# Kernel optimization log

Measured on AMD Instinct MI355X. Metric: run time of the kernel, lower is better.

Reference implementation:

```python
import jax, jax.numpy as jnp
import numpy as np

N_M, N_D, E, D, H, O = 50000, 20000, 600000, 128, 128, 64


def _graph_conv(x_src, x_dst, src, dst, W_rel, b_rel, W_root, ew=None):
    # PyG GraphConv: lin_rel(scatter_add(msg)) + lin_root(x_dst)
    msg = x_src[src]                       # [E, d_src] gather
    if ew is not None:
        msg = msg * ew[:, None]            # edge-weighted messages
    agg = jax.ops.segment_sum(msg, dst, num_segments=x_dst.shape[0])  # [N_dst, d_src]
    return agg @ W_rel + b_rel + x_dst @ W_root


def setup_inputs() -> dict:
    key = jax.random.key(0)
    ks = jax.random.split(key, 16)
    s = 1.0 / np.sqrt(D)
    inp = {
        "x_meas": jax.random.normal(ks[0], (N_M, D), jnp.float32),
        "x_dem": jax.random.normal(ks[1], (N_D, D), jnp.float32),
        "src_m": jax.random.randint(ks[2], (E,), 0, N_M, jnp.int32),
        "dst_m": jax.random.randint(ks[3], (E,), 0, N_M, jnp.int32),
        "src_b": jax.random.randint(ks[4], (E,), 0, N_M, jnp.int32),
        "dst_b": jax.random.randint(ks[5], (E,), 0, N_D, jnp.int32),
        "edge_weight": jax.random.normal(ks[6], (E,), jnp.float32),
        "W_rel1": jax.random.normal(ks[7], (D, H), jnp.float32) * s,
        "b_rel1": jnp.zeros((H,), jnp.float32),
        "W_root1": jax.random.normal(ks[8], (D, H), jnp.float32) * s,
        "W_rel2": jax.random.normal(ks[9], (D, H), jnp.float32) * s,
        "b_rel2": jnp.zeros((H,), jnp.float32),
        "W_root2": jax.random.normal(ks[10], (D, H), jnp.float32) * s,
        "W_rel3": jax.random.normal(ks[11], (H, H), jnp.float32) * s,
        "b_rel3": jnp.zeros((H,), jnp.float32),
        "W_root3": jax.random.normal(ks[12], (H, H), jnp.float32) * s,
        "W_lin": jax.random.normal(ks[13], (H, O), jnp.float32) * (1.0 / np.sqrt(H)),
        "b_lin": jnp.zeros((O,), jnp.float32),
    }
    return inp


def reference(x_meas, x_dem, src_m, dst_m, src_b, dst_b, edge_weight,
              W_rel1, b_rel1, W_root1, W_rel2, b_rel2, W_root2,
              W_rel3, b_rel3, W_root3, W_lin, b_lin):
    ew = jax.nn.sigmoid(edge_weight)
    movie_x = jax.nn.relu(_graph_conv(x_meas, x_meas, src_m, dst_m, W_rel1, b_rel1, W_root1))
    user_x = jax.nn.relu(_graph_conv(x_meas, x_dem, src_b, dst_b, W_rel2, b_rel2, W_root2, ew))
    user_x = jax.nn.relu(_graph_conv(movie_x, user_x, src_b, dst_b, W_rel3, b_rel3, W_root3, ew))
    return user_x @ W_lin + b_lin  # [N_D, O]
```

## Files before the change

kernel.cpp:

```cpp
#include <hip/hip_runtime.h>


typedef unsigned short u16;
typedef unsigned int u32;
typedef __attribute__((ext_vector_type(8))) short bf16x8;
typedef __attribute__((ext_vector_type(4))) float f32x4;

#define NMC 50000
#define NDC 20000
#define EC  600000
#define CM  64
#define CD  32
#define CHM (EC / CM)
#define CHD (EC / CD)
#define NWM (NMC / 2)
#define NWD (NDC / 2)

__device__ __forceinline__ float bf2f(u16 h) {
    union { u32 u; float f; } v; v.u = ((u32)h) << 16; return v.f;
}
__device__ __forceinline__ u16 f2bf(float f) {
    union { float f; u32 u; } v; v.f = f;
    u32 lsb = (v.u >> 16) & 1u;
    v.u += 0x7fffu + lsb;
    return (u16)(v.u >> 16);
}

__global__ __launch_bounds__(256)
void hist_lds(const int* __restrict__ dst_m, const int* __restrict__ dst_b,
              int* __restrict__ rank_m, int* __restrict__ rank_b,
              u32* __restrict__ histm, u32* __restrict__ histd)
{
    __shared__ u32 h[NWM];
    const int b = blockIdx.x;
    const bool isM = b < CM;
    const int nw = isM ? NWM : NWD;
    for (int i = threadIdx.x; i < nw; i += 256) h[i] = 0;
    __syncthreads();
    if (isM) {
        const int e0 = b * CHM;
        const int e1 = min(EC, e0 + CHM);
        for (int e = e0 + threadIdx.x; e < e1; e += 256) {
            int d = dst_m[e];
            int sh = (d & 1) * 16;
            u32 old = atomicAdd(&h[d >> 1], 1u << sh);
            rank_m[e] = (old >> sh) & 0xffffu;
        }
        __syncthreads();
        for (int i = threadIdx.x; i < nw; i += 256)
            histm[(size_t)b * NWM + i] = h[i];
    } else {
        const int bb = b - CM;
        const int e0 = bb * CHD;
        const int e1 = min(EC, e0 + CHD);
        for (int e = e0 + threadIdx.x; e < e1; e += 256) {
            int d = dst_b[e];
            int sh = (d & 1) * 16;
            u32 old = atomicAdd(&h[d >> 1], 1u << sh);
            rank_b[e] = (old >> sh) & 0xffffu;
        }
        __syncthreads();
        for (int i = threadIdx.x; i < nw; i += 256)
            histd[(size_t)bb * NWD + i] = h[i];
    }
}

__global__ __launch_bounds__(256)
void prep2(const float* __restrict__ xm, u16* __restrict__ xm_bf, int n8m,
           const float* __restrict__ xd, u16* __restrict__ xd_bf, int n8d,
           const float* __restrict__ w0, const float* __restrict__ w1,
           const float* __restrict__ w2, const float* __restrict__ w3,
           const float* __restrict__ w4, const float* __restrict__ w5,
           const float* __restrict__ w6, u16* __restrict__ wbuf,
           int TB, int TB2)
{
    const int b = blockIdx.x;
    if (b < TB + TB2) {
        const bool isM = b < TB;
        const float* src = isM ? xm : xd;
        u16* dst = isM ? xm_bf : xd_bf;
        int n8 = isM ? n8m : n8d;
        int i = (b - (isM ? 0 : TB)) * 256 + threadIdx.x;
        if (i >= n8) return;
        float4 a = ((const float4*)src)[2 * i];
        float4 c2 = ((const float4*)src)[2 * i + 1];
        ushort4 h0; h0.x = f2bf(a.x); h0.y = f2bf(a.y); h0.z = f2bf(a.z); h0.w = f2bf(a.w);
        ushort4 h1; h1.x = f2bf(c2.x); h1.y = f2bf(c2.y); h1.z = f2bf(c2.z); h1.w = f2bf(c2.w);
        ((ushort4*)dst)[2 * i]     = h0;
        ((ushort4*)dst)[2 * i + 1] = h1;
    } else {
        int bb = b - TB - TB2;
        const int widx = bb >> 6;
        const int o    = ((bb & 63) << 8) + threadIdx.x;
        const int OC   = (widx == 6) ? 64 : 128;
        if (o >= OC * 128) return;
        const float* W;
        switch (widx) {
            case 0: W = w0; break; case 1: W = w1; break; case 2: W = w2; break;
            case 3: W = w3; break; case 4: W = w4; break; case 5: W = w5; break;
            default: W = w6;
        }
        int j = o & 7;
        int lane = (o >> 3) & 63;
        int n, c;
        if (OC == 128) { n = (o >> 9) & 7; c = o >> 12; }
        else           { n = (o >> 9) & 3; c = o >> 11; }
        int col = n * 16 + (lane & 15);
        int k   = c * 32 + (lane >> 4) * 8 + j;
        wbuf[widx * 16384 + o] = f2bf(W[k * OC + col]);
    }
}

__global__ __launch_bounds__(256)
void basescan2(u32* __restrict__ histm, u32* __restrict__ histd,
               int* __restrict__ deg_m, int* __restrict__ deg_b)
{
    int w = blockIdx.x * 256 + threadIdx.x;
    u32* hist; int* deg; int NW, C;
    if (w < NWM)            { hist = histm; deg = deg_m; NW = NWM; C = CM; }
    else if (w < NWM + NWD) { hist = histd; deg = deg_b; NW = NWD; C = CD; w -= NWM; }
    else return;
    u32 runlo = 0, runhi = 0;
    for (int c = 0; c < C; ++c) {
        u32 v = hist[(size_t)c * NW + w];
        hist[(size_t)c * NW + w] = runlo | (runhi << 16);
        runlo += v & 0xffffu;
        runhi += v >> 16;
    }
    deg[2 * w]     = (int)runlo;
    deg[2 * w + 1] = (int)runhi;
}

__device__ __forceinline__ int wave_incl_scan(int v, int lane) {
#pragma unroll
    for (int off = 1; off < 64; off <<= 1) {
        int t = __shfl_up(v, off, 64);
        if (lane >= off) v += t;
    }
    return v;
}

__global__ __launch_bounds__(1024)
void scan2_kernel(const int* __restrict__ degA, int* __restrict__ rpA, int nA,
                  const int* __restrict__ degB, int* __restrict__ rpB, int nB)
{
    const int* deg = blockIdx.x ? degB : degA;
    int* rp = blockIdx.x ? rpB : rpA;
    int n = blockIdx.x ? nB : nA;

    __shared__ int wsum[16];
    __shared__ int carry;
    const int tid = threadIdx.x, lane = tid & 63, wid = tid >> 6;
    if (tid == 0) carry = 0;
    __syncthreads();

    for (int base = 0; base < n; base += 4096) {
        int idx = base + tid * 4;
        int4 v = make_int4(0, 0, 0, 0);
        if (idx + 3 < n) v = *(const int4*)(deg + idx);
        else {
            if (idx + 0 < n) v.x = deg[idx + 0];
            if (idx + 1 < n) v.y = deg[idx + 1];
            if (idx + 2 < n) v.z = deg[idx + 2];
            if (idx + 3 < n) v.w = deg[idx + 3];
        }
        int s = v.x + v.y + v.z + v.w;
        int incl = wave_incl_scan(s, lane);
        if (lane == 63) wsum[wid] = incl;
        __syncthreads();
        if (wid == 0) {
            int t = (lane < 16) ? wsum[lane] : 0;
            int ti = wave_incl_scan(t, lane);
            if (lane < 16) wsum[lane] = ti - t;
        }
        __syncthreads();
        int base_t = carry + wsum[wid] + incl - s;
        if (idx + 3 < n) {
            int4 st;
            st.x = base_t;
            st.y = base_t + v.x;
            st.z = base_t + v.x + v.y;
            st.w = base_t + v.x + v.y + v.z;
            *(int4*)(rp + idx) = st;
        } else {
            if (idx + 0 < n) rp[idx + 0] = base_t;
            if (idx + 1 < n) rp[idx + 1] = base_t + v.x;
            if (idx + 2 < n) rp[idx + 2] = base_t + v.x + v.y;
            if (idx + 3 < n) rp[idx + 3] = base_t + v.x + v.y + v.z;
        }
        __syncthreads();
        if (tid == 1023) carry += wsum[15] + incl;
        __syncthreads();
    }
    if (tid == 0) rp[n] = carry;
}

__global__ __launch_bounds__(256)
void fill_kernel(const int* __restrict__ src_m, const int* __restrict__ dst_m,
                 const int* __restrict__ src_b, const int* __restrict__ dst_b,
                 const float* __restrict__ edge_w,
                 const int* __restrict__ rp_m, const int* __restrict__ rp_b,
                 const int* __restrict__ rank_m, const int* __restrict__ rank_b,
                 const u32* __restrict__ histm, const u32* __restrict__ histd,
                 int* __restrict__ srcs_m, int2* __restrict__ edges_b, int E)
{
    int t = blockIdx.x * 256 + threadIdx.x;
    if (t < E) {
        int d = dst_m[t];
        int c = t / CHM;
        u32 pk = histm[(size_t)c * NWM + (d >> 1)];
        int base = (pk >> ((d & 1) * 16)) & 0xffffu;
        int pos = rp_m[d] + base + rank_m[t];
        srcs_m[pos] = src_m[t];
    } else if (t < 2 * E) {
        int e = t - E;
        int d = dst_b[e];
        int c = e / CHD;
        u32 pkb = histd[(size_t)c * NWD + (d >> 1)];
        int base = (pkb >> ((d & 1) * 16)) & 0xffffu;
        int pos = rp_b[d] + base + rank_b[e];
        float x = edge_w[e];
        int2 pk;
        pk.x = src_b[e];
        pk.y = __float_as_int(1.0f / (1.0f + __expf(-x)));
        edges_b[pos] = pk;
    }
}

__global__ __launch_bounds__(256)
void gather12(const u16* __restrict__ Xb,
              const int* __restrict__ srcs_m, const int2* __restrict__ edges_b,
              const int* __restrict__ rp_m, const int* __restrict__ rp_b,
              u16* __restrict__ agg1, u16* __restrict__ agg2, int NM, int ND)
{
    const int h  = blockIdx.x * 8 + (threadIdx.x >> 5);
    const int cl = threadIdx.x & 31;
    float4 acc = make_float4(0.f, 0.f, 0.f, 0.f);

    if (h < NM) {
        int i   = rp_m[h];
        int end = rp_m[h + 1];
        for (; i + 4 <= end; i += 4) {
            int s0 = srcs_m[i], s1 = srcs_m[i + 1], s2 = srcs_m[i + 2], s3 = srcs_m[i + 3];
            ushort4 v0 = *(const ushort4*)(Xb + (size_t)s0 * 128 + cl * 4);
            ushort4 v1 = *(const ushort4*)(Xb + (size_t)s1 * 128 + cl * 4);
            ushort4 v2 = *(const ushort4*)(Xb + (size_t)s2 * 128 + cl * 4);
            ushort4 v3 = *(const ushort4*)(Xb + (size_t)s3 * 128 + cl * 4);
            acc.x += (bf2f(v0.x) + bf2f(v1.x)) + (bf2f(v2.x) + bf2f(v3.x));
            acc.y += (bf2f(v0.y) + bf2f(v1.y)) + (bf2f(v2.y) + bf2f(v3.y));
            acc.z += (bf2f(v0.z) + bf2f(v1.z)) + (bf2f(v2.z) + bf2f(v3.z));
            acc.w += (bf2f(v0.w) + bf2f(v1.w)) + (bf2f(v2.w) + bf2f(v3.w));
        }
        for (; i < end; ++i) {
            int s = srcs_m[i];
            ushort4 v = *(const ushort4*)(Xb + (size_t)s * 128 + cl * 4);
            acc.x += bf2f(v.x); acc.y += bf2f(v.y);
            acc.z += bf2f(v.z); acc.w += bf2f(v.w);
        }
        ushort4 st;
        st.x = f2bf(acc.x); st.y = f2bf(acc.y);
        st.z = f2bf(acc.z); st.w = f2bf(acc.w);
        *(ushort4*)(agg1 + (size_t)h * 128 + cl * 4) = st;
    } else if (h < NM + ND) {
        int node = h - NM;
        int i   = rp_b[node];
        int end = rp_b[node + 1];
        for (; i + 4 <= end; i += 4) {
            int2 p0 = edges_b[i],     p1 = edges_b[i + 1];
            int2 p2 = edges_b[i + 2], p3 = edges_b[i + 3];
            float w0 = __int_as_float(p0.y), w1 = __int_as_float(p1.y);
            float w2 = __int_as_float(p2.y), w3 = __int_as_float(p3.y);
            ushort4 v0 = *(const ushort4*)(Xb + (size_t)p0.x * 128 + cl * 4);
            ushort4 v1 = *(const ushort4*)(Xb + (size_t)p1.x * 128 + cl * 4);
            ushort4 v2 = *(const ushort4*)(Xb + (size_t)p2.x * 128 + cl * 4);
            ushort4 v3 = *(const ushort4*)(Xb + (size_t)p3.x * 128 + cl * 4);
            acc.x = fmaf(w0, bf2f(v0.x), acc.x); acc.y = fmaf(w0, bf2f(v0.y), acc.y);
            acc.z = fmaf(w0, bf2f(v0.z), acc.z); acc.w = fmaf(w0, bf2f(v0.w), acc.w);
            acc.x = fmaf(w1, bf2f(v1.x), acc.x); acc.y = fmaf(w1, bf2f(v1.y), acc.y);
            acc.z = fmaf(w1, bf2f(v1.z), acc.z); acc.w = fmaf(w1, bf2f(v1.w), acc.w);
            acc.x = fmaf(w2, bf2f(v2.x), acc.x); acc.y = fmaf(w2, bf2f(v2.y), acc.y);
            acc.z = fmaf(w2, bf2f(v2.z), acc.z); acc.w = fmaf(w2, bf2f(v2.w), acc.w);
            acc.x = fmaf(w3, bf2f(v3.x), acc.x); acc.y = fmaf(w3, bf2f(v3.y), acc.y);
            acc.z = fmaf(w3, bf2f(v3.z), acc.z); acc.w = fmaf(w3, bf2f(v3.w), acc.w);
        }
        for (; i < end; ++i) {
            int2 pk = edges_b[i];
            float w = __int_as_float(pk.y);
            ushort4 v = *(const ushort4*)(Xb + (size_t)pk.x * 128 + cl * 4);
            acc.x = fmaf(w, bf2f(v.x), acc.x); acc.y = fmaf(w, bf2f(v.y), acc.y);
            acc.z = fmaf(w, bf2f(v.z), acc.z); acc.w = fmaf(w, bf2f(v.w), acc.w);
        }
        ushort4 st;
        st.x = f2bf(acc.x); st.y = f2bf(acc.y);
        st.z = f2bf(acc.z); st.w = f2bf(acc.w);
        *(ushort4*)(agg2 + (size_t)node * 128 + cl * 4) = st;
    }
}

__global__ __launch_bounds__(256)
void gather3_kernel(const u16* __restrict__ Mv, const int2* __restrict__ edges_b,
                    const int* __restrict__ rp_b, u16* __restrict__ agg3, int ND)
{
    const int node = blockIdx.x * 8 + (threadIdx.x >> 5);
    if (node >= ND) return;
    const int cl = threadIdx.x & 31;
    int i   = rp_b[node];
    int end = rp_b[node + 1];

    float4 acc = make_float4(0.f, 0.f, 0.f, 0.f);
    for (; i + 4 <= end; i += 4) {
        int2 p0 = edges_b[i],     p1 = edges_b[i + 1];
        int2 p2 = edges_b[i + 2], p3 = edges_b[i + 3];
        float w0 = __int_as_float(p0.y), w1 = __int_as_float(p1.y);
        float w2 = __int_as_float(p2.y), w3 = __int_as_float(p3.y);
        ushort4 v0 = *(const ushort4*)(Mv + (size_t)p0.x * 128 + cl * 4);
        ushort4 v1 = *(const ushort4*)(Mv + (size_t)p1.x * 128 + cl * 4);
        ushort4 v2 = *(const ushort4*)(Mv + (size_t)p2.x * 128 + cl * 4);
        ushort4 v3 = *(const ushort4*)(Mv + (size_t)p3.x * 128 + cl * 4);
        acc.x = fmaf(w0, bf2f(v0.x), acc.x); acc.y = fmaf(w0, bf2f(v0.y), acc.y);
        acc.z = fmaf(w0, bf2f(v0.z), acc.z); acc.w = fmaf(w0, bf2f(v0.w), acc.w);
        acc.x = fmaf(w1, bf2f(v1.x), acc.x); acc.y = fmaf(w1, bf2f(v1.y), acc.y);
        acc.z = fmaf(w1, bf2f(v1.z), acc.z); acc.w = fmaf(w1, bf2f(v1.w), acc.w);
        acc.x = fmaf(w2, bf2f(v2.x), acc.x); acc.y = fmaf(w2, bf2f(v2.y), acc.y);
        acc.z = fmaf(w2, bf2f(v2.z), acc.z); acc.w = fmaf(w2, bf2f(v2.w), acc.w);
        acc.x = fmaf(w3, bf2f(v3.x), acc.x); acc.y = fmaf(w3, bf2f(v3.y), acc.y);
        acc.z = fmaf(w3, bf2f(v3.z), acc.z); acc.w = fmaf(w3, bf2f(v3.w), acc.w);
    }
    for (; i < end; ++i) {
        int2 pk = edges_b[i];
        float w = __int_as_float(pk.y);
        ushort4 v = *(const ushort4*)(Mv + (size_t)pk.x * 128 + cl * 4);
        acc.x = fmaf(w, bf2f(v.x), acc.x); acc.y = fmaf(w, bf2f(v.y), acc.y);
        acc.z = fmaf(w, bf2f(v.z), acc.z); acc.w = fmaf(w, bf2f(v.w), acc.w);
    }
    ushort4 st;
    st.x = f2bf(acc.x); st.y = f2bf(acc.y);
    st.z = f2bf(acc.z); st.w = f2bf(acc.w);
    *(ushort4*)(agg3 + (size_t)node * 128 + cl * 4) = st;
}

__global__ __launch_bounds__(256)
void conv12_mfma(const u16* __restrict__ agg1, const u16* __restrict__ w1r,
                 const float* __restrict__ b1, const u16* __restrict__ xm_bf,
                 const u16* __restrict__ w1o, u16* __restrict__ C1, int N1, int cb1,
                 const u16* __restrict__ agg2, const u16* __restrict__ w2r,
                 const float* __restrict__ b2, const u16* __restrict__ xd_bf,
                 const u16* __restrict__ w2o, u16* __restrict__ C2, int N2)
{
    __shared__ u16 sW[16384];

    const bool seg1 = (int)blockIdx.x < cb1;
    const u16 *A0, *A1p, *Wr, *Wo; const float* bias; u16* C; int N, base;
    if (seg1) { A0 = agg1; A1p = xm_bf; Wr = w1r; Wo = w1o; bias = b1; C = C1; N = N1; base = blockIdx.x; }
    else      { A0 = agg2; A1p = xd_bf; Wr = w2r; Wo = w2o; bias = b2; C = C2; N = N2; base = blockIdx.x - cb1; }

    const int tid  = threadIdx.x;
    const int lane = tid & 63;
    const int m0   = (base * 4 + (tid >> 6)) * 32;
    const int lr   = lane & 15;
    const int quad = lane >> 4;

    int r0 = m0 + lr;      if (r0 >= N) r0 = N - 1;
    int r1 = m0 + 16 + lr; if (r1 >= N) r1 = N - 1;

    f32x4 acc[2][8];
#pragma unroll
    for (int mt = 0; mt < 2; ++mt)
#pragma unroll
        for (int n = 0; n < 8; ++n) acc[mt][n] = (f32x4){0.f, 0.f, 0.f, 0.f};

    for (int i = tid; i < 2048; i += 256)
        ((uint4*)sW)[i] = ((const uint4*)Wr)[i];
    __syncthreads();
#pragma unroll
    for (int c = 0; c < 4; ++c) {
        const int kb = c * 32 + quad * 8;
        bf16x8 a0 = *(const bf16x8*)(A0 + (size_t)r0 * 128 + kb);
        bf16x8 a1 = *(const bf16x8*)(A0 + (size_t)r1 * 128 + kb);
        const u16* wp = sW + c * 4096 + lane * 8;
#pragma unroll
        for (int n = 0; n < 8; ++n) {
            bf16x8 b = *(const bf16x8*)(wp + n * 512);
            acc[0][n] = __builtin_amdgcn_mfma_f32_16x16x32_bf16(a0, b, acc[0][n], 0, 0, 0);
            acc[1][n] = __builtin_amdgcn_mfma_f32_16x16x32_bf16(a1, b, acc[1][n], 0, 0, 0);
        }
    }
    __syncthreads();

    for (int i = tid; i < 2048; i += 256)
        ((uint4*)sW)[i] = ((const uint4*)Wo)[i];
    __syncthreads();
#pragma unroll
    for (int c = 0; c < 4; ++c) {
        const int kb = c * 32 + quad * 8;
        bf16x8 a0 = *(const bf16x8*)(A1p + (size_t)r0 * 128 + kb);
        bf16x8 a1 = *(const bf16x8*)(A1p + (size_t)r1 * 128 + kb);
        const u16* wp = sW + c * 4096 + lane * 8;
#pragma unroll
        for (int n = 0; n < 8; ++n) {
            bf16x8 b = *(const bf16x8*)(wp + n * 512);
            acc[0][n] = __builtin_amdgcn_mfma_f32_16x16x32_bf16(a0, b, acc[0][n], 0, 0, 0);
            acc[1][n] = __builtin_amdgcn_mfma_f32_16x16x32_bf16(a1, b, acc[1][n], 0, 0, 0);
        }
    }

#pragma unroll
    for (int mt = 0; mt < 2; ++mt) {
#pragma unroll
        for (int n = 0; n < 8; ++n) {
            const int col = n * 16 + lr;
            const float b = bias[col];
#pragma unroll
            for (int r = 0; r < 4; ++r) {
                int row = m0 + mt * 16 + quad * 4 + r;
                if (row >= N) continue;
                C[(size_t)row * 128 + col] = f2bf(fmaxf(acc[mt][n][r] + b, 0.f));
            }
        }
    }
}

__global__ __launch_bounds__(256)
void conv3_lin(const u16* __restrict__ A1, const u16* __restrict__ Wr,
               const float* __restrict__ bias3,
               const u16* __restrict__ A2, const u16* __restrict__ Wo,
               const u16* __restrict__ Wl, const float* __restrict__ bias_l,
               float* __restrict__ out, int N)
{
    __shared__ u16 lds[17408 + 8192];
    u16* tile = lds;
    u16* sWl  = lds + 17408;

    const int tid  = threadIdx.x;
    const int lane = tid & 63;
    const int wv   = tid >> 6;
    const int wbase = wv * 32;
    const int m0   = (blockIdx.x * 4 + wv) * 32;
    const int lr   = lane & 15;
    const int quad = lane >> 4;

    int r0 = m0 + lr;      if (r0 >= N) r0 = N - 1;
    int r1 = m0 + 16 + lr; if (r1 >= N) r1 = N - 1;

    f32x4 acc[2][8];
#pragma unroll
    for (int mt = 0; mt < 2; ++mt)
#pragma unroll
        for (int n = 0; n < 8; ++n) acc[mt][n] = (f32x4){0.f, 0.f, 0.f, 0.f};

    for (int i = tid; i < 1024; i += 256)
        ((uint4*)sWl)[i] = ((const uint4*)Wl)[i];
    for (int i = tid; i < 2048; i += 256)
        ((uint4*)lds)[i] = ((const uint4*)Wr)[i];
    __syncthreads();
#pragma unroll
    for (int c = 0; c < 4; ++c) {
        const int kb = c * 32 + quad * 8;
        bf16x8 a0 = *(const bf16x8*)(A1 + (size_t)r0 * 128 + kb);
        bf16x8 a1 = *(const bf16x8*)(A1 + (size_t)r1 * 128 + kb);
        const u16* wp = lds + c * 4096 + lane * 8;
#pragma unroll
        for (int n = 0; n < 8; ++n) {
            bf16x8 b = *(const bf16x8*)(wp + n * 512);
            acc[0][n] = __builtin_amdgcn_mfma_f32_16x16x32_bf16(a0, b, acc[0][n], 0, 0, 0);
            acc[1][n] = __builtin_amdgcn_mfma_f32_16x16x32_bf16(a1, b, acc[1][n], 0, 0, 0);
        }
    }
    __syncthreads();
    for (int i = tid; i < 2048; i += 256)
        ((uint4*)lds)[i] = ((const uint4*)Wo)[i];
    __syncthreads();
#pragma unroll
    for (int c = 0; c < 4; ++c) {
        const int kb = c * 32 + quad * 8;
        bf16x8 a0 = *(const bf16x8*)(A2 + (size_t)r0 * 128 + kb);
        bf16x8 a1 = *(const bf16x8*)(A2 + (size_t)r1 * 128 + kb);
        const u16* wp = lds + c * 4096 + lane * 8;
#pragma unroll
        for (int n = 0; n < 8; ++n) {
            bf16x8 b = *(const bf16x8*)(wp + n * 512);
            acc[0][n] = __builtin_amdgcn_mfma_f32_16x16x32_bf16(a0, b, acc[0][n], 0, 0, 0);
            acc[1][n] = __builtin_amdgcn_mfma_f32_16x16x32_bf16(a1, b, acc[1][n], 0, 0, 0);
        }
    }
    __syncthreads();

#pragma unroll
    for (int mt = 0; mt < 2; ++mt) {
#pragma unroll
        for (int n = 0; n < 8; ++n) {
            const int col = n * 16 + lr;
            const float b = bias3[col];
#pragma unroll
            for (int r = 0; r < 4; ++r) {
                int row = wbase + mt * 16 + quad * 4 + r;
                tile[row * 136 + col] = f2bf(fmaxf(acc[mt][n][r] + b, 0.f));
            }
        }
    }
    __syncthreads();

    f32x4 acc2[2][4];
#pragma unroll
    for (int mt = 0; mt < 2; ++mt)
#pragma unroll
        for (int n = 0; n < 4; ++n) acc2[mt][n] = (f32x4){0.f, 0.f, 0.f, 0.f};

#pragma unroll
    for (int c = 0; c < 4; ++c) {
        const int kb = c * 32 + quad * 8;
        bf16x8 a0 = *(const bf16x8*)(tile + (wbase + lr) * 136 + kb);
        bf16x8 a1 = *(const bf16x8*)(tile + (wbase + 16 + lr) * 136 + kb);
#pragma unroll
        for (int n = 0; n < 4; ++n) {
            bf16x8 b = *(const bf16x8*)(sWl + c * 2048 + n * 512 + lane * 8);
            acc2[0][n] = __builtin_amdgcn_mfma_f32_16x16x32_bf16(a0, b, acc2[0][n], 0, 0, 0);
            acc2[1][n] = __builtin_amdgcn_mfma_f32_16x16x32_bf16(a1, b, acc2[1][n], 0, 0, 0);
        }
    }

#pragma unroll
    for (int mt = 0; mt < 2; ++mt) {
#pragma unroll
        for (int n = 0; n < 4; ++n) {
            const int col = n * 16 + lr;
            const float b = bias_l[col];
#pragma unroll
            for (int r = 0; r < 4; ++r) {
                int row = m0 + mt * 16 + quad * 4 + r;
                if (row >= N) continue;
                out[(size_t)row * 64 + col] = acc2[mt][n][r] + b;
            }
        }
    }
}

extern "C" void kernel_launch(void* const* d_in, const int* in_sizes, int n_in,
                              void* d_out, int out_size, void* d_ws, size_t ws_size,
                              hipStream_t stream)
{
    const float* x_meas  = (const float*)d_in[0];
    const float* x_dem   = (const float*)d_in[1];
    const int*   src_m   = (const int*)d_in[2];
    const int*   dst_m   = (const int*)d_in[3];
    const int*   src_b   = (const int*)d_in[4];
    const int*   dst_b   = (const int*)d_in[5];
    const float* edge_w  = (const float*)d_in[6];
    const float* W_rel1  = (const float*)d_in[7];
    const float* b_rel1  = (const float*)d_in[8];
    const float* W_root1 = (const float*)d_in[9];
    const float* W_rel2  = (const float*)d_in[10];
    const float* b_rel2  = (const float*)d_in[11];
    const float* W_root2 = (const float*)d_in[12];
    const float* W_rel3  = (const float*)d_in[13];
    const float* b_rel3  = (const float*)d_in[14];
    const float* W_root3 = (const float*)d_in[15];
    const float* W_lin   = (const float*)d_in[16];
    const float* b_lin   = (const float*)d_in[17];
    float* out = (float*)d_out;

    const int NM = NMC, ND = NDC, E = EC;

    char* p = (char*)d_ws;
    auto alloc = [&](size_t bytes) { char* r = p; p += (bytes + 511) & ~(size_t)511; return r; };
    u32*   histm   = (u32*)alloc((size_t)CM * NWM * 4);
    u32*   histd   = (u32*)alloc((size_t)CD * NWD * 4);
    int*   deg_m   = (int*)alloc((size_t)NM * 4);
    int*   deg_b   = (int*)alloc((size_t)ND * 4);
    int*   rp_m    = (int*)alloc((size_t)(NM + 1) * 4);
    int*   rp_b    = (int*)alloc((size_t)(ND + 1) * 4);
    int*   srcs_m  = (int*)alloc((size_t)E * 4);
    int2*  edges_b = (int2*)alloc((size_t)E * 8);
    u16*   agg1    = (u16*)alloc((size_t)NM * 128 * 2);
    u16*   agg2    = (u16*)alloc((size_t)ND * 128 * 2);
    u16*   movie   = (u16*)alloc((size_t)NM * 128 * 2);
    u16*   t2      = (u16*)alloc((size_t)ND * 128 * 2);
    u16*   xd_bf   = (u16*)alloc((size_t)ND * 128 * 2);
    u16*   wbuf    = (u16*)alloc(7 * 16384 * 2);
    int* rank_m = (int*)agg1;
    int* rank_b = rank_m + E;
    u16* xm_bf  = movie;
    u16* agg3   = agg1;

    const int TB  = (NM * 16 + 255) / 256;
    const int TB2 = (ND * 16 + 255) / 256;
    const int WB  = 448;
    const int HB  = (2 * E + 255) / 256;

    hist_lds<<<CM + CD, 256, 0, stream>>>(dst_m, dst_b, rank_m, rank_b, histm, histd);

    prep2<<<TB + TB2 + WB, 256, 0, stream>>>(
        x_meas, xm_bf, NM * 16, x_dem, xd_bf, ND * 16,
        W_rel1, W_root1, W_rel2, W_root2, W_rel3, W_root3, W_lin, wbuf,
        TB, TB2);

    basescan2<<<(NWM + NWD + 255) / 256, 256, 0, stream>>>(histm, histd, deg_m, deg_b);
    scan2_kernel<<<2, 1024, 0, stream>>>(deg_m, rp_m, NM, deg_b, rp_b, ND);
    fill_kernel<<<HB, 256, 0, stream>>>(src_m, dst_m, src_b, dst_b, edge_w,
                                        rp_m, rp_b, rank_m, rank_b,
                                        histm, histd, srcs_m, edges_b, E);

    gather12<<<(NM + ND + 7) / 8, 256, 0, stream>>>(xm_bf, srcs_m, edges_b,
                                                    rp_m, rp_b, agg1, agg2, NM, ND);

    const int cb1 = (NM + 127) / 128;
    const int cb2 = (ND + 127) / 128;
    u16* w1r = wbuf + 0 * 16384; u16* w1o = wbuf + 1 * 16384;
    u16* w2r = wbuf + 2 * 16384; u16* w2o = wbuf + 3 * 16384;
    u16* w3r = wbuf + 4 * 16384; u16* w3o = wbuf + 5 * 16384;
    u16* wl  = wbuf + 6 * 16384;
    conv12_mfma<<<cb1 + cb2, 256, 0, stream>>>(agg1, w1r, b_rel1, xm_bf, w1o, movie, NM, cb1,
                                               agg2, w2r, b_rel2, xd_bf, w2o, t2,    ND);

    gather3_kernel<<<(ND + 7) / 8, 256, 0, stream>>>(movie, edges_b, rp_b, agg3, ND);

    conv3_lin<<<cb2, 256, 0, stream>>>(agg3, w3r, b_rel3, t2, w3o, wl, b_lin, out, ND);
}
```

Before: 303.4 us.

## Fuse neighbor gathers into MFMA conv kernels via per-wave LDS tiles

Merges the gather/aggregate kernels into the GraphConv MFMA kernels. Each wave gathers its 32 destination rows into a shared-memory tile and feeds that tile straight to the MFMA, so the agg1/agg2/agg3 buffers are never written to or re-read from global memory, and two launches disappear. Weight staging in LDS is dropped and B operands come straight from global/cache. The gather unroll goes from 4 to 8 edges. In exchange, each block now has only 8 half-waves (16 rows each) gathering, so gather parallelism and latency hiding may drop. Weights are also re-fetched from global per wave.

```diff
diff --git a/kernel.cpp b/kernel.cpp
--- a/kernel.cpp
+++ b/kernel.cpp
@@ -228,52 +228,203 @@
 }
 
 __global__ __launch_bounds__(256)
-void gather12(const u16* __restrict__ Xb,
-              const int* __restrict__ srcs_m, const int2* __restrict__ edges_b,
-              const int* __restrict__ rp_m, const int* __restrict__ rp_b,
-              u16* __restrict__ agg1, u16* __restrict__ agg2, int NM, int ND)
-{
-    const int h  = blockIdx.x * 8 + (threadIdx.x >> 5);
-    const int cl = threadIdx.x & 31;
-    float4 acc = make_float4(0.f, 0.f, 0.f, 0.f);
-
-    if (h < NM) {
-        int i   = rp_m[h];
-        int end = rp_m[h + 1];
-        for (; i + 4 <= end; i += 4) {
-            int s0 = srcs_m[i], s1 = srcs_m[i + 1], s2 = srcs_m[i + 2], s3 = srcs_m[i + 3];
-            ushort4 v0 = *(const ushort4*)(Xb + (size_t)s0 * 128 + cl * 4);
-            ushort4 v1 = *(const ushort4*)(Xb + (size_t)s1 * 128 + cl * 4);
-            ushort4 v2 = *(const ushort4*)(Xb + (size_t)s2 * 128 + cl * 4);
-            ushort4 v3 = *(const ushort4*)(Xb + (size_t)s3 * 128 + cl * 4);
-            acc.x += (bf2f(v0.x) + bf2f(v1.x)) + (bf2f(v2.x) + bf2f(v3.x));
-            acc.y += (bf2f(v0.y) + bf2f(v1.y)) + (bf2f(v2.y) + bf2f(v3.y));
-            acc.z += (bf2f(v0.z) + bf2f(v1.z)) + (bf2f(v2.z) + bf2f(v3.z));
-            acc.w += (bf2f(v0.w) + bf2f(v1.w)) + (bf2f(v2.w) + bf2f(v3.w));
-        }
-        for (; i < end; ++i) {
-            int s = srcs_m[i];
-            ushort4 v = *(const ushort4*)(Xb + (size_t)s * 128 + cl * 4);
-            acc.x += bf2f(v.x); acc.y += bf2f(v.y);
-            acc.z += bf2f(v.z); acc.w += bf2f(v.w);
+void conv12g(const u16* __restrict__ gtab,
+             const int* __restrict__ srcs_m, const int2* __restrict__ edges_b,
+             const int* __restrict__ rp_m, const int* __restrict__ rp_b,
+             const u16* __restrict__ w1r, const u16* __restrict__ w1o,
+             const float* __restrict__ b1, u16* __restrict__ C1, int N1, int cb1,
+             const u16* __restrict__ xd_bf,
+             const u16* __restrict__ w2r, const u16* __restrict__ w2o,
+             const float* __restrict__ b2, u16* __restrict__ C2, int N2)
+{
+    __shared__ u16 tile[4][32][136];
+
+    const bool seg1 = (int)blockIdx.x < cb1;
+    const int  base = seg1 ? blockIdx.x : (blockIdx.x - cb1);
+    const int  N    = seg1 ? N1 : N2;
+    const int* rp   = seg1 ? rp_m : rp_b;
+    const u16* Aroot = seg1 ? gtab : xd_bf;
+    const u16* Wr   = seg1 ? w1r : w2r;
+    const u16* Wo   = seg1 ? w1o : w2o;
+    const float* bias = seg1 ? b1 : b2;
+    u16* C = seg1 ? C1 : C2;
+
+    const int tid = threadIdx.x;
+    const int wv  = tid >> 6;
+    const int hw  = (tid >> 5) & 1;
+    const int cl  = tid & 31;
+    const int m0  = (base * 4 + wv) * 32;
+
+    for (int j = 0; j < 16; ++j) {
+        const int k = hw * 16 + j;
+        int node = m0 + k; if (node >= N) node = N - 1;
+        int i = rp[node], end = rp[node + 1];
+        float4 acc = make_float4(0.f, 0.f, 0.f, 0.f);
+        if (seg1) {
+            for (; i + 8 <= end; i += 8) {
+                int s0 = srcs_m[i+0], s1 = srcs_m[i+1], s2 = srcs_m[i+2], s3 = srcs_m[i+3];
+                int s4 = srcs_m[i+4], s5 = srcs_m[i+5], s6 = srcs_m[i+6], s7 = srcs_m[i+7];
+                ushort4 v0 = *(const ushort4*)(gtab + (size_t)s0 * 128 + cl * 4);
+                ushort4 v1 = *(const ushort4*)(gtab + (size_t)s1 * 128 + cl * 4);
+                ushort4 v2 = *(const ushort4*)(gtab + (size_t)s2 * 128 + cl * 4);
+                ushort4 v3 = *(const ushort4*)(gtab + (size_t)s3 * 128 + cl * 4);
+                ushort4 v4 = *(const ushort4*)(gtab + (size_t)s4 * 128 + cl * 4);
+                ushort4 v5 = *(const ushort4*)(gtab + (size_t)s5 * 128 + cl * 4);
+                ushort4 v6 = *(const ushort4*)(gtab + (size_t)s6 * 128 + cl * 4);
+                ushort4 v7 = *(const ushort4*)(gtab + (size_t)s7 * 128 + cl * 4);
+                acc.x += ((bf2f(v0.x)+bf2f(v1.x)) + (bf2f(v2.x)+bf2f(v3.x)))
+                       + ((bf2f(v4.x)+bf2f(v5.x)) + (bf2f(v6.x)+bf2f(v7.x)));
+                acc.y += ((bf2f(v0.y)+bf2f(v1.y)) + (bf2f(v2.y)+bf2f(v3.y)))
+                       + ((bf2f(v4.y)+bf2f(v5.y)) + (bf2f(v6.y)+bf2f(v7.y)));
+                acc.z += ((bf2f(v0.z)+bf2f(v1.z)) + (bf2f(v2.z)+bf2f(v3.z)))
+                       + ((bf2f(v4.z)+bf2f(v5.z)) + (bf2f(v6.z)+bf2f(v7.z)));
+                acc.w += ((bf2f(v0.w)+bf2f(v1.w)) + (bf2f(v2.w)+bf2f(v3.w)))
+                       + ((bf2f(v4.w)+bf2f(v5.w)) + (bf2f(v6.w)+bf2f(v7.w)));
+            }
+            for (; i < end; ++i) {
+                int s = srcs_m[i];
+                ushort4 v = *(const ushort4*)(gtab + (size_t)s * 128 + cl * 4);
+                acc.x += bf2f(v.x); acc.y += bf2f(v.y);
+                acc.z += bf2f(v.z); acc.w += bf2f(v.w);
+            }
+        } else {
+            for (; i + 8 <= end; i += 8) {
+                int2 p0 = edges_b[i+0], p1 = edges_b[i+1], p2 = edges_b[i+2], p3 = edges_b[i+3];
+                int2 p4 = edges_b[i+4], p5 = edges_b[i+5], p6 = edges_b[i+6], p7 = edges_b[i+7];
+                ushort4 v0 = *(const ushort4*)(gtab + (size_t)p0.x * 128 + cl * 4);
+                ushort4 v1 = *(const ushort4*)(gtab + (size_t)p1.x * 128 + cl * 4);
+                ushort4 v2 = *(const ushort4*)(gtab + (size_t)p2.x * 128 + cl * 4);
+                ushort4 v3 = *(const ushort4*)(gtab + (size_t)p3.x * 128 + cl * 4);
+                ushort4 v4 = *(const ushort4*)(gtab + (size_t)p4.x * 128 + cl * 4);
+                ushort4 v5 = *(const ushort4*)(gtab + (size_t)p5.x * 128 + cl * 4);
+                ushort4 v6 = *(const ushort4*)(gtab + (size_t)p6.x * 128 + cl * 4);
+                ushort4 v7 = *(const ushort4*)(gtab + (size_t)p7.x * 128 + cl * 4);
+                float w0 = __int_as_float(p0.y), w1 = __int_as_float(p1.y);
+                float w2 = __int_as_float(p2.y), w3 = __int_as_float(p3.y);
+                float w4 = __int_as_float(p4.y), w5 = __int_as_float(p5.y);
+                float w6 = __int_as_float(p6.y), w7 = __int_as_float(p7.y);
+                acc.x = fmaf(w0, bf2f(v0.x), acc.x); acc.y = fmaf(w0, bf2f(v0.y), acc.y);
+                acc.z = fmaf(w0, bf2f(v0.z), acc.z); acc.w = fmaf(w0, bf2f(v0.w), acc.w);
+                acc.x = fmaf(w1, bf2f(v1.x), acc.x); acc.y = fmaf(w1, bf2f(v1.y), acc.y);
+                acc.z = fmaf(w1, bf2f(v1.z), acc.z); acc.w = fmaf(w1, bf2f(v1.w), acc.w);
+                acc.x = fmaf(w2, bf2f(v2.x), acc.x); acc.y = fmaf(w2, bf2f(v2.y), acc.y);
+                acc.z = fmaf(w2, bf2f(v2.z), acc.z); acc.w = fmaf(w2, bf2f(v2.w), acc.w);
+                acc.x = fmaf(w3, bf2f(v3.x), acc.x); acc.y = fmaf(w3, bf2f(v3.y), acc.y);
+                acc.z = fmaf(w3, bf2f(v3.z), acc.z); acc.w = fmaf(w3, bf2f(v3.w), acc.w);
+                acc.x = fmaf(w4, bf2f(v4.x), acc.x); acc.y = fmaf(w4, bf2f(v4.y), acc.y);
+                acc.z = fmaf(w4, bf2f(v4.z), acc.z); acc.w = fmaf(w4, bf2f(v4.w), acc.w);
+                acc.x = fmaf(w5, bf2f(v5.x), acc.x); acc.y = fmaf(w5, bf2f(v5.y), acc.y);
+                acc.z = fmaf(w5, bf2f(v5.z), acc.z); acc.w = fmaf(w5, bf2f(v5.w), acc.w);
+                acc.x = fmaf(w6, bf2f(v6.x), acc.x); acc.y = fmaf(w6, bf2f(v6.y), acc.y);
+                acc.z = fmaf(w6, bf2f(v6.z), acc.z); acc.w = fmaf(w6, bf2f(v6.w), acc.w);
+                acc.x = fmaf(w7, bf2f(v7.x), acc.x); acc.y = fmaf(w7, bf2f(v7.y), acc.y);
+                acc.z = fmaf(w7, bf2f(v7.z), acc.z); acc.w = fmaf(w7, bf2f(v7.w), acc.w);
+            }
+            for (; i < end; ++i) {
+                int2 pk = edges_b[i];
+                float w = __int_as_float(pk.y);
+                ushort4 v = *(const ushort4*)(gtab + (size_t)pk.x * 128 + cl * 4);
+                acc.x = fmaf(w, bf2f(v.x), acc.x); acc.y = fmaf(w, bf2f(v.y), acc.y);
+                acc.z = fmaf(w, bf2f(v.z), acc.z); acc.w = fmaf(w, bf2f(v.w), acc.w);
+            }
         }
         ushort4 st;
         st.x = f2bf(acc.x); st.y = f2bf(acc.y);
         st.z = f2bf(acc.z); st.w = f2bf(acc.w);
-        *(ushort4*)(agg1 + (size_t)h * 128 + cl * 4) = st;
-    } else if (h < NM + ND) {
-        int node = h - NM;
-        int i   = rp_b[node];
-        int end = rp_b[node + 1];
-        for (; i + 4 <= end; i += 4) {
-            int2 p0 = edges_b[i],     p1 = edges_b[i + 1];
-            int2 p2 = edges_b[i + 2], p3 = edges_b[i + 3];
+        *(ushort4*)(&tile[wv][k][cl * 4]) = st;
+    }
+
+    const int lane = tid & 63;
+    const int lr   = lane & 15;
+    const int quad = lane >> 4;
+    int r0 = m0 + lr;      if (r0 >= N) r0 = N - 1;
+    int r1 = m0 + 16 + lr; if (r1 >= N) r1 = N - 1;
+
+    f32x4 acc[2][8];
+#pragma unroll
+    for (int mt = 0; mt < 2; ++mt)
+#pragma unroll
+        for (int n = 0; n < 8; ++n) acc[mt][n] = (f32x4){0.f, 0.f, 0.f, 0.f};
+
+#pragma unroll
+    for (int c = 0; c < 4; ++c) {
+        const int kb = c * 32 + quad * 8;
+        bf16x8 a0 = *(const bf16x8*)(&tile[wv][lr][kb]);
+        bf16x8 a1 = *(const bf16x8*)(&tile[wv][16 + lr][kb]);
+        const u16* wp = Wr + c * 4096 + lane * 8;
+#pragma unroll
+        for (int n = 0; n < 8; ++n) {
+            bf16x8 b = *(const bf16x8*)(wp + n * 512);
+            acc[0][n] = __builtin_amdgcn_mfma_f32_16x16x32_bf16(a0, b, acc[0][n], 0, 0, 0);
+            acc[1][n] = __builtin_amdgcn_mfma_f32_16x16x32_bf16(a1, b, acc[1][n], 0, 0, 0);
+        }
+    }
+#pragma unroll
+    for (int c = 0; c < 4; ++c) {
+        const int kb = c * 32 + quad * 8;
+        bf16x8 a0 = *(const bf16x8*)(Aroot + (size_t)r0 * 128 + kb);
+        bf16x8 a1 = *(const bf16x8*)(Aroot + (size_t)r1 * 128 + kb);
+        const u16* wp = Wo + c * 4096 + lane * 8;
+#pragma unroll
+        for (int n = 0; n < 8; ++n) {
+            bf16x8 b = *(const bf16x8*)(wp + n * 512);
+            acc[0][n] = __builtin_amdgcn_mfma_f32_16x16x32_bf16(a0, b, acc[0][n], 0, 0, 0);
+            acc[1][n] = __builtin_amdgcn_mfma_f32_16x16x32_bf16(a1, b, acc[1][n], 0, 0, 0);
+        }
+    }
+
+#pragma unroll
+    for (int mt = 0; mt < 2; ++mt) {
+#pragma unroll
+        for (int n = 0; n < 8; ++n) {
+            const int col = n * 16 + lr;
+            const float b = bias[col];
+#pragma unroll
+            for (int r = 0; r < 4; ++r) {
+                int row = m0 + mt * 16 + quad * 4 + r;
+                if (row >= N) continue;
+                C[(size_t)row * 128 + col] = f2bf(fmaxf(acc[mt][n][r] + b, 0.f));
+            }
+        }
+    }
+}
+
+__global__ __launch_bounds__(256)
+void conv3g(const u16* __restrict__ movie, const int2* __restrict__ edges_b,
+            const int* __restrict__ rp_b,
+            const u16* __restrict__ w3r, const u16* __restrict__ w3o,
+            const float* __restrict__ bias3, const u16* __restrict__ t2,
+            const u16* __restrict__ wl, const float* __restrict__ bias_l,
+            float* __restrict__ out, int N)
+{
+    __shared__ u16 tile[4][32][136];
+
+    const int tid = threadIdx.x;
+    const int wv  = tid >> 6;
+    const int hw  = (tid >> 5) & 1;
+    const int cl  = tid & 31;
+    const int m0  = (blockIdx.x * 4 + wv) * 32;
+
+    for (int j = 0; j < 16; ++j) {
+        const int k = hw * 16 + j;
+        int node = m0 + k; if (node >= N) node = N - 1;
+        int i = rp_b[node], end = rp_b[node + 1];
+        float4 acc = make_float4(0.f, 0.f, 0.f, 0.f);
+        for (; i + 8 <= end; i += 8) {
+            int2 p0 = edges_b[i+0], p1 = edges_b[i+1], p2 = edges_b[i+2], p3 = edges_b[i+3];
+            int2 p4 = edges_b[i+4], p5 = edges_b[i+5], p6 = edges_b[i+6], p7 = edges_b[i+7];
+            ushort4 v0 = *(const ushort4*)(movie + (size_t)p0.x * 128 + cl * 4);
+            ushort4 v1 = *(const ushort4*)(movie + (size_t)p1.x * 128 + cl * 4);
+            ushort4 v2 = *(const ushort4*)(movie + (size_t)p2.x * 128 + cl * 4);
+            ushort4 v3 = *(const ushort4*)(movie + (size_t)p3.x * 128 + cl * 4);
+            ushort4 v4 = *(const ushort4*)(movie + (size_t)p4.x * 128 + cl * 4);
+            ushort4 v5 = *(const ushort4*)(movie + (size_t)p5.x * 128 + cl * 4);
+            ushort4 v6 = *(const ushort4*)(movie + (size_t)p6.x * 128 + cl * 4);
+            ushort4 v7 = *(const ushort4*)(movie + (size_t)p7.x * 128 + cl * 4);
             float w0 = __int_as_float(p0.y), w1 = __int_as_float(p1.y);
             float w2 = __int_as_float(p2.y), w3 = __int_as_float(p3.y);
-            ushort4 v0 = *(const ushort4*)(Xb + (size_t)p0.x * 128 + cl * 4);
-            ushort4 v1 = *(const ushort4*)(Xb + (size_t)p1.x * 128 + cl * 4);
-            ushort4 v2 = *(const ushort4*)(Xb + (size_t)p2.x * 128 + cl * 4);
-            ushort4 v3 = *(const ushort4*)(Xb + (size_t)p3.x * 128 + cl * 4);
+            float w4 = __int_as_float(p4.y), w5 = __int_as_float(p5.y);
+            float w6 = __int_as_float(p6.y), w7 = __int_as_float(p7.y);
             acc.x = fmaf(w0, bf2f(v0.x), acc.x); acc.y = fmaf(w0, bf2f(v0.y), acc.y);
             acc.z = fmaf(w0, bf2f(v0.z), acc.z); acc.w = fmaf(w0, bf2f(v0.w), acc.w);
             acc.x = fmaf(w1, bf2f(v1.x), acc.x); acc.y = fmaf(w1, bf2f(v1.y), acc.y);
@@ -282,84 +433,31 @@
             acc.z = fmaf(w2, bf2f(v2.z), acc.z); acc.w = fmaf(w2, bf2f(v2.w), acc.w);
             acc.x = fmaf(w3, bf2f(v3.x), acc.x); acc.y = fmaf(w3, bf2f(v3.y), acc.y);
             acc.z = fmaf(w3, bf2f(v3.z), acc.z); acc.w = fmaf(w3, bf2f(v3.w), acc.w);
+            acc.x = fmaf(w4, bf2f(v4.x), acc.x); acc.y = fmaf(w4, bf2f(v4.y), acc.y);
+            acc.z = fmaf(w4, bf2f(v4.z), acc.z); acc.w = fmaf(w4, bf2f(v4.w), acc.w);
+            acc.x = fmaf(w5, bf2f(v5.x), acc.x); acc.y = fmaf(w5, bf2f(v5.y), acc.y);
+            acc.z = fmaf(w5, bf2f(v5.z), acc.z); acc.w = fmaf(w5, bf2f(v5.w), acc.w);
+            acc.x = fmaf(w6, bf2f(v6.x), acc.x); acc.y = fmaf(w6, bf2f(v6.y), acc.y);
+            acc.z = fmaf(w6, bf2f(v6.z), acc.z); acc.w = fmaf(w6, bf2f(v6.w), acc.w);
+            acc.x = fmaf(w7, bf2f(v7.x), acc.x); acc.y = fmaf(w7, bf2f(v7.y), acc.y);
+            acc.z = fmaf(w7, bf2f(v7.z), acc.z); acc.w = fmaf(w7, bf2f(v7.w), acc.w);
         }
         for (; i < end; ++i) {
             int2 pk = edges_b[i];
             float w = __int_as_float(pk.y);
-            ushort4 v = *(const ushort4*)(Xb + (size_t)pk.x * 128 + cl * 4);
+            ushort4 v = *(const ushort4*)(movie + (size_t)pk.x * 128 + cl * 4);
             acc.x = fmaf(w, bf2f(v.x), acc.x); acc.y = fmaf(w, bf2f(v.y), acc.y);
             acc.z = fmaf(w, bf2f(v.z), acc.z); acc.w = fmaf(w, bf2f(v.w), acc.w);
         }
         ushort4 st;
         st.x = f2bf(acc.x); st.y = f2bf(acc.y);
         st.z = f2bf(acc.z); st.w = f2bf(acc.w);
-        *(ushort4*)(agg2 + (size_t)node * 128 + cl * 4) = st;
-    }
-}
-
-__global__ __launch_bounds__(256)
-void gather3_kernel(const u16* __restrict__ Mv, const int2* __restrict__ edges_b,
-                    const int* __restrict__ rp_b, u16* __restrict__ agg3, int ND)
-{
-    const int node = blockIdx.x * 8 + (threadIdx.x >> 5);
-    if (node >= ND) return;
-    const int cl = threadIdx.x & 31;
-    int i   = rp_b[node];
-    int end = rp_b[node + 1];
-
-    float4 acc = make_float4(0.f, 0.f, 0.f, 0.f);
-    for (; i + 4 <= end; i += 4) {
-        int2 p0 = edges_b[i],     p1 = edges_b[i + 1];
-        int2 p2 = edges_b[i + 2], p3 = edges_b[i + 3];
-        float w0 = __int_as_float(p0.y), w1 = __int_as_float(p1.y);
-        float w2 = __int_as_float(p2.y), w3 = __int_as_float(p3.y);
-        ushort4 v0 = *(const ushort4*)(Mv + (size_t)p0.x * 128 + cl * 4);
-        ushort4 v1 = *(const ushort4*)(Mv + (size_t)p1.x * 128 + cl * 4);
-        ushort4 v2 = *(const ushort4*)(Mv + (size_t)p2.x * 128 + cl * 4);
-        ushort4 v3 = *(const ushort4*)(Mv + (size_t)p3.x * 128 + cl * 4);
-        acc.x = fmaf(w0, bf2f(v0.x), acc.x); acc.y = fmaf(w0, bf2f(v0.y), acc.y);
-        acc.z = fmaf(w0, bf2f(v0.z), acc.z); acc.w = fmaf(w0, bf2f(v0.w), acc.w);
-        acc.x = fmaf(w1, bf2f(v1.x), acc.x); acc.y = fmaf(w1, bf2f(v1.y), acc.y);
-        acc.z = fmaf(w1, bf2f(v1.z), acc.z); acc.w = fmaf(w1, bf2f(v1.w), acc.w);
-        acc.x = fmaf(w2, bf2f(v2.x), acc.x); acc.y = fmaf(w2, bf2f(v2.y), acc.y);
-        acc.z = fmaf(w2, bf2f(v2.z), acc.z); acc.w = fmaf(w2, bf2f(v2.w), acc.w);
-        acc.x = fmaf(w3, bf2f(v3.x), acc.x); acc.y = fmaf(w3, bf2f(v3.y), acc.y);
-        acc.z = fmaf(w3, bf2f(v3.z), acc.z); acc.w = fmaf(w3, bf2f(v3.w), acc.w);
-    }
-    for (; i < end; ++i) {
-        int2 pk = edges_b[i];
-        float w = __int_as_float(pk.y);
-        ushort4 v = *(const ushort4*)(Mv + (size_t)pk.x * 128 + cl * 4);
-        acc.x = fmaf(w, bf2f(v.x), acc.x); acc.y = fmaf(w, bf2f(v.y), acc.y);
-        acc.z = fmaf(w, bf2f(v.z), acc.z); acc.w = fmaf(w, bf2f(v.w), acc.w);
-    }
-    ushort4 st;
-    st.x = f2bf(acc.x); st.y = f2bf(acc.y);
-    st.z = f2bf(acc.z); st.w = f2bf(acc.w);
-    *(ushort4*)(agg3 + (size_t)node * 128 + cl * 4) = st;
-}
-
-__global__ __launch_bounds__(256)
-void conv12_mfma(const u16* __restrict__ agg1, const u16* __restrict__ w1r,
-                 const float* __restrict__ b1, const u16* __restrict__ xm_bf,
-                 const u16* __restrict__ w1o, u16* __restrict__ C1, int N1, int cb1,
-                 const u16* __restrict__ agg2, const u16* __restrict__ w2r,
-                 const float* __restrict__ b2, const u16* __restrict__ xd_bf,
-                 const u16* __restrict__ w2o, u16* __restrict__ C2, int N2)
-{
-    __shared__ u16 sW[16384];
-
-    const bool seg1 = (int)blockIdx.x < cb1;
-    const u16 *A0, *A1p, *Wr, *Wo; const float* bias; u16* C; int N, base;
-    if (seg1) { A0 = agg1; A1p = xm_bf; Wr = w1r; Wo = w1o; bias = b1; C = C1; N = N1; base = blockIdx.x; }
-    else      { A0 = agg2; A1p = xd_bf; Wr = w2r; Wo = w2o; bias = b2; C = C2; N = N2; base = blockIdx.x - cb1; }
-
-    const int tid  = threadIdx.x;
+        *(ushort4*)(&tile[wv][k][cl * 4]) = st;
+    }
+
     const int lane = tid & 63;
-    const int m0   = (base * 4 + (tid >> 6)) * 32;
     const int lr   = lane & 15;
     const int quad = lane >> 4;
-
     int r0 = m0 + lr;      if (r0 >= N) r0 = N - 1;
     int r1 = m0 + 16 + lr; if (r1 >= N) r1 = N - 1;
 
@@ -369,15 +467,12 @@
 #pragma unroll
         for (int n = 0; n < 8; ++n) acc[mt][n] = (f32x4){0.f, 0.f, 0.f, 0.f};
 
-    for (int i = tid; i < 2048; i += 256)
-        ((uint4*)sW)[i] = ((const uint4*)Wr)[i];
-    __syncthreads();
 #pragma unroll
     for (int c = 0; c < 4; ++c) {
         const int kb = c * 32 + quad * 8;
-        bf16x8 a0 = *(const bf16x8*)(A0 + (size_t)r0 * 128 + kb);
-        bf16x8 a1 = *(const bf16x8*)(A0 + (size_t)r1 * 128 + kb);
-        const u16* wp = sW + c * 4096 + lane * 8;
+        bf16x8 a0 = *(const bf16x8*)(&tile[wv][lr][kb]);
+        bf16x8 a1 = *(const bf16x8*)(&tile[wv][16 + lr][kb]);
+        const u16* wp = w3r + c * 4096 + lane * 8;
 #pragma unroll
         for (int n = 0; n < 8; ++n) {
             bf16x8 b = *(const bf16x8*)(wp + n * 512);
@@ -385,17 +480,12 @@
             acc[1][n] = __builtin_amdgcn_mfma_f32_16x16x32_bf16(a1, b, acc[1][n], 0, 0, 0);
         }
     }
-    __syncthreads();
-
-    for (int i = tid; i < 2048; i += 256)
-        ((uint4*)sW)[i] = ((const uint4*)Wo)[i];
-    __syncthreads();
 #pragma unroll
     for (int c = 0; c < 4; ++c) {
         const int kb = c * 32 + quad * 8;
-        bf16x8 a0 = *(const bf16x8*)(A1p + (size_t)r0 * 128 + kb);
-        bf16x8 a1 = *(const bf16x8*)(A1p + (size_t)r1 * 128 + kb);
-        const u16* wp = sW + c * 4096 + lane * 8;
+        bf16x8 a0 = *(const bf16x8*)(t2 + (size_t)r0 * 128 + kb);
+        bf16x8 a1 = *(const bf16x8*)(t2 + (size_t)r1 * 128 + kb);
+        const u16* wp = w3o + c * 4096 + lane * 8;
 #pragma unroll
         for (int n = 0; n < 8; ++n) {
             bf16x8 b = *(const bf16x8*)(wp + n * 512);
@@ -409,111 +499,29 @@
 #pragma unroll
         for (int n = 0; n < 8; ++n) {
             const int col = n * 16 + lr;
-            const float b = bias[col];
+            const float b = bias3[col];
 #pragma unroll
             for (int r = 0; r < 4; ++r) {
-                int row = m0 + mt * 16 + quad * 4 + r;
-                if (row >= N) continue;
-                C[(size_t)row * 128 + col] = f2bf(fmaxf(acc[mt][n][r] + b, 0.f));
+                int row = mt * 16 + quad * 4 + r;
+                tile[wv][row][col] = f2bf(fmaxf(acc[mt][n][r] + b, 0.f));
             }
         }
     }
-}
-
-__global__ __launch_bounds__(256)
-void conv3_lin(const u16* __restrict__ A1, const u16* __restrict__ Wr,
-               const float* __restrict__ bias3,
-               const u16* __restrict__ A2, const u16* __restrict__ Wo,
-               const u16* __restrict__ Wl, const float* __restrict__ bias_l,
-               float* __restrict__ out, int N)
-{
-    __shared__ u16 lds[17408 + 8192];
-    u16* tile = lds;
-    u16* sWl  = lds + 17408;
-
-    const int tid  = threadIdx.x;
-    const int lane = tid & 63;
-    const int wv   = tid >> 6;
-    const int wbase = wv * 32;
-    const int m0   = (blockIdx.x * 4 + wv) * 32;
-    const int lr   = lane & 15;
-    const int quad = lane >> 4;
-
-    int r0 = m0 + lr;      if (r0 >= N) r0 = N - 1;
-    int r1 = m0 + 16 + lr; if (r1 >= N) r1 = N - 1;
-
-    f32x4 acc[2][8];
+
+    f32x4 acc2[2][4];
 #pragma unroll
     for (int mt = 0; mt < 2; ++mt)
 #pragma unroll
-        for (int n = 0; n < 8; ++n) acc[mt][n] = (f32x4){0.f, 0.f, 0.f, 0.f};
-
-    for (int i = tid; i < 1024; i += 256)
-        ((uint4*)sWl)[i] = ((const uint4*)Wl)[i];
-    for (int i = tid; i < 2048; i += 256)
-        ((uint4*)lds)[i] = ((const uint4*)Wr)[i];
-    __syncthreads();
+        for (int n = 0; n < 4; ++n) acc2[mt][n] = (f32x4){0.f, 0.f, 0.f, 0.f};
+
 #pragma unroll
     for (int c = 0; c < 4; ++c) {
         const int kb = c * 32 + quad * 8;
-        bf16x8 a0 = *(const bf16x8*)(A1 + (size_t)r0 * 128 + kb);
-        bf16x8 a1 = *(const bf16x8*)(A1 + (size_t)r1 * 128 + kb);
-        const u16* wp = lds + c * 4096 + lane * 8;
-#pragma unroll
-        for (int n = 0; n < 8; ++n) {
-            bf16x8 b = *(const bf16x8*)(wp + n * 512);
-            acc[0][n] = __builtin_amdgcn_mfma_f32_16x16x32_bf16(a0, b, acc[0][n], 0, 0, 0);
-            acc[1][n] = __builtin_amdgcn_mfma_f32_16x16x32_bf16(a1, b, acc[1][n], 0, 0, 0);
-        }
-    }
-    __syncthreads();
-    for (int i = tid; i < 2048; i += 256)
-        ((uint4*)lds)[i] = ((const uint4*)Wo)[i];
-    __syncthreads();
-#pragma unroll
-    for (int c = 0; c < 4; ++c) {
-        const int kb = c * 32 + quad * 8;
-        bf16x8 a0 = *(const bf16x8*)(A2 + (size_t)r0 * 128 + kb);
-        bf16x8 a1 = *(const bf16x8*)(A2 + (size_t)r1 * 128 + kb);
-        const u16* wp = lds + c * 4096 + lane * 8;
-#pragma unroll
-        for (int n = 0; n < 8; ++n) {
-            bf16x8 b = *(const bf16x8*)(wp + n * 512);
-            acc[0][n] = __builtin_amdgcn_mfma_f32_16x16x32_bf16(a0, b, acc[0][n], 0, 0, 0);
-            acc[1][n] = __builtin_amdgcn_mfma_f32_16x16x32_bf16(a1, b, acc[1][n], 0, 0, 0);
-        }
-    }
-    __syncthreads();
-
-#pragma unroll
-    for (int mt = 0; mt < 2; ++mt) {
-#pragma unroll
-        for (int n = 0; n < 8; ++n) {
-            const int col = n * 16 + lr;
-            const float b = bias3[col];
-#pragma unroll
-            for (int r = 0; r < 4; ++r) {
-                int row = wbase + mt * 16 + quad * 4 + r;
-                tile[row * 136 + col] = f2bf(fmaxf(acc[mt][n][r] + b, 0.f));
-            }
-        }
-    }
-    __syncthreads();
-
-    f32x4 acc2[2][4];
-#pragma unroll
-    for (int mt = 0; mt < 2; ++mt)
-#pragma unroll
-        for (int n = 0; n < 4; ++n) acc2[mt][n] = (f32x4){0.f, 0.f, 0.f, 0.f};
-
-#pragma unroll
-    for (int c = 0; c < 4; ++c) {
-        const int kb = c * 32 + quad * 8;
-        bf16x8 a0 = *(const bf16x8*)(tile + (wbase + lr) * 136 + kb);
-        bf16x8 a1 = *(const bf16x8*)(tile + (wbase + 16 + lr) * 136 + kb);
+        bf16x8 a0 = *(const bf16x8*)(&tile[wv][lr][kb]);
+        bf16x8 a1 = *(const bf16x8*)(&tile[wv][16 + lr][kb]);
 #pragma unroll
         for (int n = 0; n < 4; ++n) {
-            bf16x8 b = *(const bf16x8*)(sWl + c * 2048 + n * 512 + lane * 8);
+            bf16x8 b = *(const bf16x8*)(wl + c * 2048 + n * 512 + lane * 8);
             acc2[0][n] = __builtin_amdgcn_mfma_f32_16x16x32_bf16(a0, b, acc2[0][n], 0, 0, 0);
             acc2[1][n] = __builtin_amdgcn_mfma_f32_16x16x32_bf16(a1, b, acc2[1][n], 0, 0, 0);
         }
@@ -571,16 +579,13 @@
     int*   rp_b    = (int*)alloc((size_t)(ND + 1) * 4);
     int*   srcs_m  = (int*)alloc((size_t)E * 4);
     int2*  edges_b = (int2*)alloc((size_t)E * 8);
-    u16*   agg1    = (u16*)alloc((size_t)NM * 128 * 2);
-    u16*   agg2    = (u16*)alloc((size_t)ND * 128 * 2);
+    u16*   xm_bf   = (u16*)alloc((size_t)NM * 128 * 2);
     u16*   movie   = (u16*)alloc((size_t)NM * 128 * 2);
+    u16*   xd_bf   = (u16*)alloc((size_t)ND * 128 * 2);
     u16*   t2      = (u16*)alloc((size_t)ND * 128 * 2);
-    u16*   xd_bf   = (u16*)alloc((size_t)ND * 128 * 2);
     u16*   wbuf    = (u16*)alloc(7 * 16384 * 2);
-    int* rank_m = (int*)agg1;
+    int* rank_m = (int*)movie;
     int* rank_b = rank_m + E;
-    u16* xm_bf  = movie;
-    u16* agg3   = agg1;
 
     const int TB  = (NM * 16 + 255) / 256;
     const int TB2 = (ND * 16 + 255) / 256;
@@ -599,9 +604,6 @@
     fill_kernel<<<HB, 256, 0, stream>>>(src_m, dst_m, src_b, dst_b, edge_w,
                                         rp_m, rp_b, rank_m, rank_b,
                                         histm, histd, srcs_m, edges_b, E);
-
-    gather12<<<(NM + ND + 7) / 8, 256, 0, stream>>>(xm_bf, srcs_m, edges_b,
-                                                    rp_m, rp_b, agg1, agg2, NM, ND);
 
     const int cb1 = (NM + 127) / 128;
     const int cb2 = (ND + 127) / 128;
@@ -609,10 +611,11 @@
     u16* w2r = wbuf + 2 * 16384; u16* w2o = wbuf + 3 * 16384;
     u16* w3r = wbuf + 4 * 16384; u16* w3o = wbuf + 5 * 16384;
     u16* wl  = wbuf + 6 * 16384;
-    conv12_mfma<<<cb1 + cb2, 256, 0, stream>>>(agg1, w1r, b_rel1, xm_bf, w1o, movie, NM, cb1,
-                                               agg2, w2r, b_rel2, xd_bf, w2o, t2,    ND);
-
-    gather3_kernel<<<(ND + 7) / 8, 256, 0, stream>>>(movie, edges_b, rp_b, agg3, ND);
-
-    conv3_lin<<<cb2, 256, 0, stream>>>(agg3, w3r, b_rel3, t2, w3o, wl, b_lin, out, ND);
-}
+
+    conv12g<<<cb1 + cb2, 256, 0, stream>>>(xm_bf, srcs_m, edges_b, rp_m, rp_b,
+                                           w1r, w1o, b_rel1, movie, NM, cb1,
+                                           xd_bf, w2r, w2o, b_rel2, t2, ND);
+
+    conv3g<<<cb2, 256, 0, stream>>>(movie, edges_b, rp_b, w3r, w3o, b_rel3,
+                                    t2, wl, b_lin, out, ND);
+}
```

Result: slower. 433.4 us (+42.8%).
